# Performance work log

Hardware: AMD Instinct MI355X
Metric: run time of the kernel (lower is better)

## Reference

```python
import jax, jax.numpy as jnp
import numpy as np

SCALE = 1.0 / np.sqrt(64.0)  # module hardcodes 64**0.5, independent of d


def setup_inputs() -> dict:
    key = jax.random.key(0)
    k1, k2 = jax.random.split(key)
    x = jax.random.normal(k1, (8, 2048, 512), dtype=jnp.float32)
    kernel = jax.random.normal(k2, (3, 512, 512), dtype=jnp.float32) * 0.02
    return {"x": x, "kernel": kernel}


def reference(x, kernel):
    # x: [b, s, d]; kernel: [3, d, d]
    q = jnp.einsum('bsd,de->bse', x, kernel[0])
    k = jnp.einsum('bsd,de->bse', x, kernel[1])
    v = jnp.einsum('bsd,de->bse', x, kernel[2])
    scores = jnp.einsum('bqd,bkd->bqk', q, k) * SCALE  # [b, s, s]
    attn = jax.nn.softmax(scores, axis=-1)
    return jnp.einsum('bqk,bkd->bqd', attn, v)
```

## Files before the change

kernel.cpp:

```cpp
#include <hip/hip_runtime.h>


typedef unsigned short u16;
typedef unsigned int u32;

using bf16x8 = __attribute__((ext_vector_type(8))) short;
using f32x4  = __attribute__((ext_vector_type(4))) float;
using u16x4  = __attribute__((ext_vector_type(4))) u16;

__device__ __forceinline__ u16 f2bf(float f) {
  u32 u = __float_as_uint(f);
  u32 r = (u + 0x7FFFu + ((u >> 16) & 1u)) >> 16;
  return (u16)r;
}
__device__ __forceinline__ float bf2f(u16 h) {
  return __uint_as_float(((u32)h) << 16);
}

#define GLL16(src, dst)                                                        \
  __builtin_amdgcn_global_load_lds(                                            \
      (const __attribute__((address_space(1))) void*)(src),                    \
      (__attribute__((address_space(3))) void*)(dst), 16, 0, 0)

template <int K, bool ROWSUM_MFMA>
__device__ __forceinline__ void gemm8p_256x128(
    const u16* __restrict__ A0, const u16* __restrict__ B0,
    u16* lds, f32x4 (&acc)[4][4], f32x4* acc5)
{
  const int tid = threadIdx.x;
  const int w = tid >> 6, l = tid & 63;
  const int wm = w >> 1, wn = w & 1;
  const int fr = l & 15;
  const int laneChunk = ((l >> 4) ^ ((fr >> 1) & 3)) << 3;
  const int laneA = (wm * 64 + fr) * 32 + laneChunk;
  const int laneB = (wn * 64 + fr) * 32 + laneChunk;
  u16* const ldsA = lds;
  u16* const ldsB = lds + 24576;

  const int chunkS = ((tid & 3) ^ ((tid >> 3) & 3)) << 3;
  const int r0 = tid >> 2;
  const u16* const sA0 = A0 + (size_t)r0 * K + chunkS;
  const u16* const sA1 = A0 + (size_t)(r0 + 128) * K + chunkS;
  const u16* const sB0 = B0 + (size_t)r0 * K + chunkS;
  const int dOf = w * 512;

  bf16x8 bOnes;
#pragma unroll
  for (int i = 0; i < 8; ++i) bOnes[i] = (short)0x3F80;

#define PSTAGE_A(j, slot) do {                                                 \
    u16* d_ = ldsA + (slot) * 8192 + dOf;                                      \
    GLL16(sA0 + (j) * 32, d_);                                                 \
    GLL16(sA1 + (j) * 32, d_ + 4096);                                          \
  } while (0)
#define PSTAGE_B(j, slot) do {                                                 \
    u16* d_ = ldsB + (slot) * 4096 + dOf;                                      \
    GLL16(sB0 + (j) * 32, d_);                                                 \
  } while (0)

  PSTAGE_B(0, 0); PSTAGE_A(0, 0);
  PSTAGE_B(1, 1); PSTAGE_A(1, 1);

  constexpr int NS = K / 32;
  int slot = 0;
  for (int j = 0; j < NS; ++j) {
    const int jn = (j + 2 < NS) ? (j + 2) : (NS - 1);
    int slotn = slot + 2; if (slotn >= 3) slotn -= 3;

    asm volatile("s_waitcnt vmcnt(3)\n\ts_barrier" ::: "memory");

    const u16* const Ab = ldsA + slot * 8192;
    const u16* const Bb = ldsB + slot * 4096;
    bf16x8 a[4], b[4];
#pragma unroll
    for (int i = 0; i < 4; ++i) a[i] = *(const bf16x8*)(Ab + laneA + i * 512);
#pragma unroll
    for (int i = 0; i < 4; ++i) b[i] = *(const bf16x8*)(Bb + laneB + i * 512);
    PSTAGE_B(jn, slotn);
    __builtin_amdgcn_s_setprio(1);
#pragma unroll
    for (int mi = 0; mi < 2; ++mi)
#pragma unroll
      for (int nj = 0; nj < 4; ++nj)
        acc[mi][nj] = __builtin_amdgcn_mfma_f32_16x16x32_bf16(a[mi], b[nj], acc[mi][nj], 0, 0, 0);
    __builtin_amdgcn_s_setprio(0);
    PSTAGE_A(jn, slotn);
    __builtin_amdgcn_s_setprio(1);
#pragma unroll
    for (int mi = 2; mi < 4; ++mi)
#pragma unroll
      for (int nj = 0; nj < 4; ++nj)
        acc[mi][nj] = __builtin_amdgcn_mfma_f32_16x16x32_bf16(a[mi], b[nj], acc[mi][nj], 0, 0, 0);
    if (ROWSUM_MFMA) {
#pragma unroll
      for (int mi = 0; mi < 4; ++mi)
        acc5[mi] = __builtin_amdgcn_mfma_f32_16x16x32_bf16(a[mi], bOnes, acc5[mi], 0, 0, 0);
    }
    __builtin_amdgcn_s_setprio(0);

    slot = (slot == 2) ? 0 : slot + 1;
  }
#undef PSTAGE_A
#undef PSTAGE_B
}

template <int K>
__device__ __forceinline__ void gemm8p_256sq_pp(
    const u16* __restrict__ A0, const u16* __restrict__ B0,
    u16* lds, f32x4 (&acc)[8][4])
{
  const int tid = threadIdx.x;
  const int w = tid >> 6, l = tid & 63;
  const int wm = w >> 2, wn = w & 3;
  const int fr = l & 15;
  const int laneChunk = ((l >> 4) ^ ((fr >> 1) & 3)) << 3;
  const int laneA = (wm * 128 + fr) * 32 + laneChunk;
  const int laneB = (wn * 64 + fr) * 32 + laneChunk;
  u16* const ldsA = lds;
  u16* const ldsB = lds + 24576;

  const int chunkS = ((tid & 3) ^ ((tid >> 3) & 3)) << 3;
  const int r0 = tid >> 2;
  const u16* const sA0 = A0 + (size_t)r0 * K + chunkS;
  const u16* const sA1 = A0 + (size_t)(r0 + 128) * K + chunkS;
  const u16* const sB0 = B0 + (size_t)r0 * K + chunkS;
  const u16* const sB1 = B0 + (size_t)(r0 + 128) * K + chunkS;
  const int dOf = w * 512;

#define SSTAGE_A(j, slot) do {                                                 \
    u16* d_ = ldsA + (slot) * 8192 + dOf;                                      \
    GLL16(sA0 + (j) * 32, d_);                                                 \
    GLL16(sA1 + (j) * 32, d_ + 4096);                                          \
  } while (0)
#define SSTAGE_B(j, slot) do {                                                 \
    u16* d_ = ldsB + (slot) * 8192 + dOf;                                      \
    GLL16(sB0 + (j) * 32, d_);                                                 \
    GLL16(sB1 + (j) * 32, d_ + 4096);                                          \
  } while (0)

  constexpr int NS = K / 32;
  bf16x8 bP[4], aP0[4], aP1[4], bQ[4], aQ0[4], aQ1[4];

  SSTAGE_B(0, 0); SSTAGE_A(0, 0);
  SSTAGE_B(1, 1); SSTAGE_A(1, 1);
  SSTAGE_B(2, 2); SSTAGE_A(2, 2);
  asm volatile("s_waitcnt vmcnt(8)\n\ts_barrier" ::: "memory");
#pragma unroll
  for (int i = 0; i < 4; ++i) bP[i]  = *(const bf16x8*)(ldsB + laneB + i * 512);
#pragma unroll
  for (int i = 0; i < 4; ++i) aP0[i] = *(const bf16x8*)(ldsA + laneA + i * 512);
#pragma unroll
  for (int i = 0; i < 4; ++i) aP1[i] = *(const bf16x8*)(ldsA + laneA + (4 + i) * 512);

#define SITER(jj, CB, CA0, CA1, NB, NA0, NA1) do {                             \
    const int js_ = ((jj) + 3 < NS) ? (jj) + 3 : NS - 1;                       \
    const int sS_ = (jj) % 3;                                                  \
    const int sR_ = ((jj) + 1) % 3;                                            \
    asm volatile("s_waitcnt vmcnt(4) lgkmcnt(0)\n\ts_barrier" ::: "memory");   \
    const u16* const Ab_ = ldsA + sR_ * 8192;                                  \
    const u16* const Bb_ = ldsB + sR_ * 8192;                                  \
    _Pragma("unroll")                                                          \
    for (int i = 0; i < 4; ++i) NB[i]  = *(const bf16x8*)(Bb_ + laneB + i * 512); \
    _Pragma("unroll")                                                          \
    for (int i = 0; i < 4; ++i) NA0[i] = *(const bf16x8*)(Ab_ + laneA + i * 512); \
    SSTAGE_A(js_, sS_);                                                        \
    __builtin_amdgcn_s_setprio(1);                                             \
    _Pragma("unroll")                                                          \
    for (int mi = 0; mi < 4; ++mi)                                             \
      _Pragma("unroll")                                                        \
      for (int nj = 0; nj < 4; ++nj)                                           \
        acc[mi][nj] = __builtin_amdgcn_mfma_f32_16x16x32_bf16(                 \
            CA0[mi], CB[nj], acc[mi][nj], 0, 0, 0);                            \
    __builtin_amdgcn_s_setprio(0);                                             \
    _Pragma("unroll")                                                          \
    for (int i = 0; i < 4; ++i) NA1[i] = *(const bf16x8*)(Ab_ + laneA + (4 + i) * 512); \
    SSTAGE_B(js_, sS_);                                                        \
    __builtin_amdgcn_s_setprio(1);                                             \
    _Pragma("unroll")                                                          \
    for (int mi = 0; mi < 4; ++mi)                                             \
      _Pragma("unroll")                                                        \
      for (int nj = 0; nj < 4; ++nj)                                           \
        acc[4 + mi][nj] = __builtin_amdgcn_mfma_f32_16x16x32_bf16(             \
            CA1[mi], CB[nj], acc[4 + mi][nj], 0, 0, 0);                        \
    __builtin_amdgcn_s_setprio(0);                                             \
  } while (0)

  for (int j = 0; j < NS; j += 2) {
    SITER(j, bP, aP0, aP1, bQ, aQ0, aQ1);
    SITER(j + 1, bQ, aQ0, aQ1, bP, aP0, aP1);
  }
#undef SITER
#undef SSTAGE_A
#undef SSTAGE_B
}


__global__ void convert_x_kernel(const float* __restrict__ x, u16* __restrict__ xb) {
  int i = blockIdx.x * 256 + threadIdx.x;
  float4 f = ((const float4*)x)[i];
  u16x4 o = { f2bf(f.x), f2bf(f.y), f2bf(f.z), f2bf(f.w) };
  ((u16x4*)xb)[i] = o;
}

__global__ void convw_kernel(const float* __restrict__ W, u16* __restrict__ wT) {
  __shared__ float tile[32][33];
  const int mtx = blockIdx.z;
  const int e0 = blockIdx.x * 32, d0 = blockIdx.y * 32;
  const int tx = threadIdx.x, ty = threadIdx.y;
  const float* Wm = W + (size_t)mtx * 262144;
#pragma unroll
  for (int i = 0; i < 32; i += 8)
    tile[ty + i][tx] = Wm[(size_t)(d0 + ty + i) * 512 + e0 + tx];
  __syncthreads();
  u16* T = wT + (size_t)mtx * 262144;
#pragma unroll
  for (int i = 0; i < 32; i += 8)
    T[(size_t)(e0 + ty + i) * 512 + d0 + tx] = f2bf(tile[tx][ty + i]);
}

__global__ __launch_bounds__(512, 4) void gemm_qkv128_kernel(
    const u16* __restrict__ xb, const u16* __restrict__ wT,
    u16* __restrict__ qb, u16* __restrict__ kb, u16* __restrict__ vt)
{
  __shared__ __align__(16) u16 lds[36864];
  const int id = blockIdx.x;
  const int xcd = id & 7, t = id >> 3;
  const int n0 = (t % 12) * 128;
  const int m0 = (xcd * 8 + t / 12) * 256;
  f32x4 acc[4][4] = {};
  gemm8p_256x128<512, false>(xb + (size_t)m0 * 512, wT + (size_t)n0 * 512, lds, acc, nullptr);

  const int tid = threadIdx.x, w = tid >> 6, l = tid & 63;
  const int wm = w >> 1, wn = w & 1;
  const int which = n0 >> 9;
  const int eb = (n0 & 511) + wn * 64 + (l & 15);
  const int rb = m0 + wm * 64 + (l >> 4) * 4;
  if (which < 2) {
    u16* dst = which ? kb : qb;
#pragma unroll
    for (int mi = 0; mi < 4; ++mi)
#pragma unroll
      for (int nj = 0; nj < 4; ++nj) {
        const int row = rb + mi * 16;
        const int col = eb + nj * 16;
#pragma unroll
        for (int r = 0; r < 4; ++r)
          dst[(size_t)(row + r) * 512 + col] = f2bf(acc[mi][nj][r]);
      }
  } else {
#pragma unroll
    for (int mi = 0; mi < 4; ++mi)
#pragma unroll
      for (int nj = 0; nj < 4; ++nj) {
        const int s = rb + mi * 16;
        const int b = s >> 11, sl = s & 2047;
        const int e = eb + nj * 16;
        u16x4 pk;
#pragma unroll
        for (int r = 0; r < 4; ++r) pk[r] = f2bf(acc[mi][nj][r]);
        *(u16x4*)(vt + (size_t)b * 1048576 + (size_t)e * 2048 + sl) = pk;
      }
  }
}

__global__ __launch_bounds__(512, 2) void gemm_scores256_kernel(
    const u16* __restrict__ qb, const u16* __restrict__ kb, u16* __restrict__ attn)
{
  __shared__ __align__(16) u16 lds[49152];
  const int id = blockIdx.x;
  const int z = id & 7, t = id >> 3;
  const int n0 = (t & 7) * 256;
  const int m0 = (t >> 3) * 256;
  f32x4 acc[8][4] = {};
  gemm8p_256sq_pp<512>(qb + (size_t)z * 1048576 + (size_t)m0 * 512,
                       kb + (size_t)z * 1048576 + (size_t)n0 * 512, lds, acc);

  const int tid = threadIdx.x, w = tid >> 6, l = tid & 63;
  const int wm = w >> 2, wn = w & 3;
  u16* C = attn + (size_t)z * 4194304;
  const int rb = m0 + wm * 128 + (l >> 4) * 4;
  const int cb = n0 + wn * 64 + (l & 15);
#pragma unroll
  for (int mi = 0; mi < 8; ++mi)
#pragma unroll
    for (int nj = 0; nj < 4; ++nj) {
      const int row = rb + mi * 16;
      const int col = cb + nj * 16;
#pragma unroll
      for (int r = 0; r < 4; ++r)
        C[(size_t)(row + r) * 2048 + col] = f2bf(__expf(acc[mi][nj][r] * 0.125f));
    }
}

__global__ __launch_bounds__(512, 2) void gemm_pv8p_kernel(
    const u16* __restrict__ attn, const u16* __restrict__ vt, float* __restrict__ out)
{
  __shared__ __align__(16) u16 lds[36864];
  const int id = blockIdx.x;
  const int z = id & 7;
  const int j = id >> 3;
  const int n0 = (j & 3) * 128;
  const int m0 = (j >> 2) * 256;
  f32x4 acc[4][4] = {};
  f32x4 acc5[4] = {};
  gemm8p_256x128<2048, true>(attn + (size_t)z * 4194304 + (size_t)m0 * 2048,
                             vt + (size_t)z * 1048576 + (size_t)n0 * 2048, lds, acc, acc5);

  const int tid = threadIdx.x, w = tid >> 6, l = tid & 63;
  const int wm = w >> 1, wn = w & 1;
  const int rb = m0 + wm * 64 + (l >> 4) * 4;
  const int cb = n0 + wn * 64 + (l & 15);
  float* C = out + (size_t)z * 1048576;
#pragma unroll
  for (int mi = 0; mi < 4; ++mi)
#pragma unroll
    for (int r = 0; r < 4; ++r) {
      const float inv = 1.f / acc5[mi][r];
      const int row = rb + mi * 16 + r;
#pragma unroll
      for (int nj = 0; nj < 4; ++nj)
        C[(size_t)row * 512 + cb + nj * 16] = acc[mi][nj][r] * inv;
    }
}

extern "C" void kernel_launch(void* const* d_in, const int* in_sizes, int n_in,
                              void* d_out, int out_size, void* d_ws, size_t ws_size,
                              hipStream_t stream) {
  const float* x = (const float*)d_in[0];
  const float* W = (const float*)d_in[1];
  float* out = (float*)d_out;

  if (ws_size < 117440512) return;
  u16* wsu  = (u16*)d_ws;
  u16* qb   = wsu;
  u16* kb   = qb + 8388608;
  u16* vt   = kb + 8388608;
  u16* attn = vt + 8388608;
  u16* xb   = attn;
  u16* wT   = attn + 8388608;

  convert_x_kernel<<<8192, 256, 0, stream>>>(x, xb);
  convw_kernel<<<dim3(16, 16, 3), dim3(32, 8), 0, stream>>>(W, wT);
  gemm_qkv128_kernel<<<768, 512, 0, stream>>>(xb, wT, qb, kb, vt);
  gemm_scores256_kernel<<<512, 512, 0, stream>>>(qb, kb, attn);
  gemm_pv8p_kernel<<<256, 512, 0, stream>>>(attn, vt, out);
}
```

Baseline: 126.0 us.

## Use four-slot LDS ring with ping-pong register fragments in scores and PV GEMMs

Both the scores GEMM and the PV GEMM move from a three-slot to a four-slot LDS ring buffer. Slot indexing now uses a bitmask instead of modulo, and the lgkmcnt(0) wait is dropped from the per-iteration barrier. The PV GEMM gets a new software-pipelined loop that double-buffers its A/B register fragments, loading the next k-step from LDS while the current step's MFMAs run, with the ones-vector row-sum MFMA folded in. This should hide more LDS and global latency, but it raises LDS usage per block, which could lower occupancy, and the deeper ring adds risk of WAR hazards between slots.

```diff
diff --git a/kernel.cpp b/kernel.cpp
--- a/kernel.cpp
+++ b/kernel.cpp
@@ -22,10 +22,10 @@
       (const __attribute__((address_space(1))) void*)(src),                    \
       (__attribute__((address_space(3))) void*)(dst), 16, 0, 0)
 
-template <int K, bool ROWSUM_MFMA>
+template <int K>
 __device__ __forceinline__ void gemm8p_256x128(
     const u16* __restrict__ A0, const u16* __restrict__ B0,
-    u16* lds, f32x4 (&acc)[4][4], f32x4* acc5)
+    u16* lds, f32x4 (&acc)[4][4])
 {
   const int tid = threadIdx.x;
   const int w = tid >> 6, l = tid & 63;
@@ -44,10 +44,6 @@
   const u16* const sB0 = B0 + (size_t)r0 * K + chunkS;
   const int dOf = w * 512;
 
-  bf16x8 bOnes;
-#pragma unroll
-  for (int i = 0; i < 8; ++i) bOnes[i] = (short)0x3F80;
-
 #define PSTAGE_A(j, slot) do {                                                 \
     u16* d_ = ldsA + (slot) * 8192 + dOf;                                      \
     GLL16(sA0 + (j) * 32, d_);                                                 \
@@ -91,11 +87,6 @@
 #pragma unroll
       for (int nj = 0; nj < 4; ++nj)
         acc[mi][nj] = __builtin_amdgcn_mfma_f32_16x16x32_bf16(a[mi], b[nj], acc[mi][nj], 0, 0, 0);
-    if (ROWSUM_MFMA) {
-#pragma unroll
-      for (int mi = 0; mi < 4; ++mi)
-        acc5[mi] = __builtin_amdgcn_mfma_f32_16x16x32_bf16(a[mi], bOnes, acc5[mi], 0, 0, 0);
-    }
     __builtin_amdgcn_s_setprio(0);
 
     slot = (slot == 2) ? 0 : slot + 1;
@@ -105,7 +96,99 @@
 }
 
 template <int K>
-__device__ __forceinline__ void gemm8p_256sq_pp(
+__device__ __forceinline__ void gemm128_pp4(
+    const u16* __restrict__ A0, const u16* __restrict__ B0,
+    u16* lds, f32x4 (&acc)[4][4], f32x4 (&acc5)[4])
+{
+  const int tid = threadIdx.x;
+  const int w = tid >> 6, l = tid & 63;
+  const int wm = w >> 1, wn = w & 1;
+  const int fr = l & 15;
+  const int laneChunk = ((l >> 4) ^ ((fr >> 1) & 3)) << 3;
+  const int laneA = (wm * 64 + fr) * 32 + laneChunk;
+  const int laneB = (wn * 64 + fr) * 32 + laneChunk;
+  u16* const ldsA = lds;
+  u16* const ldsB = lds + 32768;
+
+  const int chunkS = ((tid & 3) ^ ((tid >> 3) & 3)) << 3;
+  const int r0 = tid >> 2;
+  const u16* const sA0 = A0 + (size_t)r0 * K + chunkS;
+  const u16* const sA1 = A0 + (size_t)(r0 + 128) * K + chunkS;
+  const u16* const sB0 = B0 + (size_t)r0 * K + chunkS;
+  const int dOf = w * 512;
+
+  bf16x8 bOnes;
+#pragma unroll
+  for (int i = 0; i < 8; ++i) bOnes[i] = (short)0x3F80;
+
+#define PSTAGE_A(j, slot) do {                                                 \
+    u16* d_ = ldsA + (slot) * 8192 + dOf;                                      \
+    GLL16(sA0 + (j) * 32, d_);                                                 \
+    GLL16(sA1 + (j) * 32, d_ + 4096);                                          \
+  } while (0)
+#define PSTAGE_B(j, slot) do {                                                 \
+    u16* d_ = ldsB + (slot) * 4096 + dOf;                                      \
+    GLL16(sB0 + (j) * 32, d_);                                                 \
+  } while (0)
+
+  constexpr int NS = K / 32;
+  bf16x8 aP[4], bP[4], aQ[4], bQ[4];
+
+  PSTAGE_B(0, 0); PSTAGE_A(0, 0);
+  PSTAGE_B(1, 1); PSTAGE_A(1, 1);
+  PSTAGE_B(2, 2); PSTAGE_A(2, 2);
+  asm volatile("s_waitcnt vmcnt(6)\n\ts_barrier" ::: "memory");
+#pragma unroll
+  for (int i = 0; i < 4; ++i) aP[i] = *(const bf16x8*)(ldsA + laneA + i * 512);
+#pragma unroll
+  for (int i = 0; i < 4; ++i) bP[i] = *(const bf16x8*)(ldsB + laneB + i * 512);
+
+#define KITER(jj, CA, CB, NA, NB) do {                                         \
+    const int js_ = ((jj) + 3 < NS) ? (jj) + 3 : NS - 1;                       \
+    const int sS_ = ((jj) + 3) & 3;                                            \
+    const int sR_ = ((jj) + 1) & 3;                                            \
+    asm volatile("s_waitcnt vmcnt(3)\n\ts_barrier" ::: "memory");              \
+    const u16* const Ab_ = ldsA + sR_ * 8192;                                  \
+    const u16* const Bb_ = ldsB + sR_ * 4096;                                  \
+    _Pragma("unroll")                                                          \
+    for (int i = 0; i < 4; ++i) NB[i] = *(const bf16x8*)(Bb_ + laneB + i * 512); \
+    _Pragma("unroll")                                                          \
+    for (int i = 0; i < 4; ++i) NA[i] = *(const bf16x8*)(Ab_ + laneA + i * 512); \
+    PSTAGE_B(js_, sS_);                                                        \
+    __builtin_amdgcn_s_setprio(1);                                             \
+    _Pragma("unroll")                                                          \
+    for (int mi = 0; mi < 2; ++mi)                                             \
+      _Pragma("unroll")                                                        \
+      for (int nj = 0; nj < 4; ++nj)                                           \
+        acc[mi][nj] = __builtin_amdgcn_mfma_f32_16x16x32_bf16(                 \
+            CA[mi], CB[nj], acc[mi][nj], 0, 0, 0);                             \
+    __builtin_amdgcn_s_setprio(0);                                             \
+    PSTAGE_A(js_, sS_);                                                        \
+    __builtin_amdgcn_s_setprio(1);                                             \
+    _Pragma("unroll")                                                          \
+    for (int mi = 2; mi < 4; ++mi)                                             \
+      _Pragma("unroll")                                                        \
+      for (int nj = 0; nj < 4; ++nj)                                           \
+        acc[mi][nj] = __builtin_amdgcn_mfma_f32_16x16x32_bf16(                 \
+            CA[mi], CB[nj], acc[mi][nj], 0, 0, 0);                             \
+    _Pragma("unroll")                                                          \
+    for (int mi = 0; mi < 4; ++mi)                                             \
+      acc5[mi] = __builtin_amdgcn_mfma_f32_16x16x32_bf16(                      \
+          CA[mi], bOnes, acc5[mi], 0, 0, 0);                                   \
+    __builtin_amdgcn_s_setprio(0);                                             \
+  } while (0)
+
+  for (int j = 0; j < NS; j += 2) {
+    KITER(j, aP, bP, aQ, bQ);
+    KITER(j + 1, aQ, bQ, aP, bP);
+  }
+#undef KITER
+#undef PSTAGE_A
+#undef PSTAGE_B
+}
+
+template <int K>
+__device__ __forceinline__ void gemm8p_256sq_pp4(
     const u16* __restrict__ A0, const u16* __restrict__ B0,
     u16* lds, f32x4 (&acc)[8][4])
 {
@@ -117,7 +200,7 @@
   const int laneA = (wm * 128 + fr) * 32 + laneChunk;
   const int laneB = (wn * 64 + fr) * 32 + laneChunk;
   u16* const ldsA = lds;
-  u16* const ldsB = lds + 24576;
+  u16* const ldsB = lds + 32768;
 
   const int chunkS = ((tid & 3) ^ ((tid >> 3) & 3)) << 3;
   const int r0 = tid >> 2;
@@ -154,9 +237,9 @@
 
 #define SITER(jj, CB, CA0, CA1, NB, NA0, NA1) do {                             \
     const int js_ = ((jj) + 3 < NS) ? (jj) + 3 : NS - 1;                       \
-    const int sS_ = (jj) % 3;                                                  \
-    const int sR_ = ((jj) + 1) % 3;                                            \
-    asm volatile("s_waitcnt vmcnt(4) lgkmcnt(0)\n\ts_barrier" ::: "memory");   \
+    const int sS_ = ((jj) + 3) & 3;                                            \
+    const int sR_ = ((jj) + 1) & 3;                                            \
+    asm volatile("s_waitcnt vmcnt(4)\n\ts_barrier" ::: "memory");              \
     const u16* const Ab_ = ldsA + sR_ * 8192;                                  \
     const u16* const Bb_ = ldsB + sR_ * 8192;                                  \
     _Pragma("unroll")                                                          \
@@ -228,7 +311,7 @@
   const int n0 = (t % 12) * 128;
   const int m0 = (xcd * 8 + t / 12) * 256;
   f32x4 acc[4][4] = {};
-  gemm8p_256x128<512, false>(xb + (size_t)m0 * 512, wT + (size_t)n0 * 512, lds, acc, nullptr);
+  gemm8p_256x128<512>(xb + (size_t)m0 * 512, wT + (size_t)n0 * 512, lds, acc);
 
   const int tid = threadIdx.x, w = tid >> 6, l = tid & 63;
   const int wm = w >> 1, wn = w & 1;
@@ -266,14 +349,14 @@
 __global__ __launch_bounds__(512, 2) void gemm_scores256_kernel(
     const u16* __restrict__ qb, const u16* __restrict__ kb, u16* __restrict__ attn)
 {
-  __shared__ __align__(16) u16 lds[49152];
+  __shared__ __align__(16) u16 lds[65536];
   const int id = blockIdx.x;
   const int z = id & 7, t = id >> 3;
   const int n0 = (t & 7) * 256;
   const int m0 = (t >> 3) * 256;
   f32x4 acc[8][4] = {};
-  gemm8p_256sq_pp<512>(qb + (size_t)z * 1048576 + (size_t)m0 * 512,
-                       kb + (size_t)z * 1048576 + (size_t)n0 * 512, lds, acc);
+  gemm8p_256sq_pp4<512>(qb + (size_t)z * 1048576 + (size_t)m0 * 512,
+                        kb + (size_t)z * 1048576 + (size_t)n0 * 512, lds, acc);
 
   const int tid = threadIdx.x, w = tid >> 6, l = tid & 63;
   const int wm = w >> 2, wn = w & 3;
@@ -295,7 +378,7 @@
 __global__ __launch_bounds__(512, 2) void gemm_pv8p_kernel(
     const u16* __restrict__ attn, const u16* __restrict__ vt, float* __restrict__ out)
 {
-  __shared__ __align__(16) u16 lds[36864];
+  __shared__ __align__(16) u16 lds[49152];
   const int id = blockIdx.x;
   const int z = id & 7;
   const int j = id >> 3;
@@ -303,8 +386,8 @@
   const int m0 = (j >> 2) * 256;
   f32x4 acc[4][4] = {};
   f32x4 acc5[4] = {};
-  gemm8p_256x128<2048, true>(attn + (size_t)z * 4194304 + (size_t)m0 * 2048,
-                             vt + (size_t)z * 1048576 + (size_t)n0 * 2048, lds, acc, acc5);
+  gemm128_pp4<2048>(attn + (size_t)z * 4194304 + (size_t)m0 * 2048,
+                    vt + (size_t)z * 1048576 + (size_t)n0 * 2048, lds, acc, acc5);
 
   const int tid = threadIdx.x, w = tid >> 6, l = tid & 63;
   const int wm = w >> 1, wn = w & 1;
```

After: 124.0 us. About the same (-1.6%).
